# Optimization experiments

Hardware: AMD Instinct MI355X
Metric: run time of the kernel (lower is better)

The kernel has to match this reference:

```python
import jax, jax.numpy as jnp
from jax import lax
import numpy as np


def setup_inputs() -> dict:
    key = jax.random.key(0)
    ks = jax.random.split(key, 7)
    B, C, L, H, K = 64, 256, 2048, 8, 3
    return {
        "src": jax.random.normal(ks[0], (B, C, L), dtype=jnp.float32),
        "conv_w": jax.random.normal(ks[1], (H, C, K), dtype=jnp.float32) * 0.05,
        "conv_b": jax.random.normal(ks[2], (H,), dtype=jnp.float32) * 0.05,
        "bn_gamma": jnp.ones((H,), dtype=jnp.float32),
        "bn_beta": jnp.zeros((H,), dtype=jnp.float32),
        "comb_w": jax.random.normal(ks[5], (H,), dtype=jnp.float32) * 0.3,
        "comb_b": jax.random.normal(ks[6], (1,), dtype=jnp.float32) * 0.05,
        "k": 64,
    }


def reference(src, conv_w, conv_b, bn_gamma, bn_beta, comb_w, comb_b, k):
    # src: (B, C, L); conv_w: (H, C, K)
    B, C, L = src.shape
    H, _, K = conv_w.shape
    # att_conv: valid 1D conv -> (B, H, Lp), Lp = L - K + 1
    xi = lax.conv_general_dilated(src, conv_w, (1,), 'VALID',
                                  dimension_numbers=('NCH', 'OIH', 'NCH'))
    xi = xi + conv_b[None, :, None]
    # BatchNorm1d in the original runs on a batch of 1 (training mode), so
    # stats are per-sample over the length dim; biased var, eps = 1e-5.
    mu = jnp.mean(xi, axis=2, keepdims=True)
    var = jnp.var(xi, axis=2, keepdims=True)
    xn = (xi - mu) * lax.rsqrt(var + 1e-5) * bn_gamma[None, :, None] + bn_beta[None, :, None]
    Lp = xn.shape[2]
    # per-(b, h) top-k indicator; indices are detached (.data) in the original
    _, idx = lax.top_k(xn, k)  # (B, H, k)
    bidx = jnp.arange(B)[:, None, None]
    hidx = jnp.arange(H)[None, :, None]
    ind = jnp.zeros_like(xn).at[bidx, hidx, idx].set(1.0)  # (B, H, Lp)
    m = jax.nn.sigmoid(xn) * ind  # softmask, (B, H, Lp)
    # kernel_size-way shifted-padding sum: M[b,h,l] = sum_i m[b,h,l-i] -> (B, H, L)
    M = sum(jnp.pad(m, ((0, 0), (0, 0), (i, K - 1 - i))) for i in range(K))
    # combine_conv is a 1x1 conv over heads; since softmasked_src[h,c,l] =
    # src[c,l] * M[h,l] / K, the head mix commutes with the src broadcast:
    gate = jnp.einsum('h,bhl->bl', comb_w, M) / K  # (B, L)
    return src * gate[:, None, :] + comb_b[0]  # (B, C, L)
```

## Files before the change

kernel.cpp:

```cpp
#include <hip/hip_runtime.h>
#include <hip/hip_bf16.h>

#define NB 64
#define NC 256
#define NL 2048
#define NH 8
#define KW 3
#define LP (NL - KW + 1)
#define NCHUNK 8
#define CPC (NC / NCHUNK)

typedef float v4f __attribute__((ext_vector_type(4)));

__device__ __forceinline__ unsigned fkey(float x) {
  unsigned b = __float_as_uint(x);
  return (b & 0x80000000u) ? ~b : (b | 0x80000000u);
}

__global__ __launch_bounds__(256) void conv_partial(
    const float* __restrict__ src, const float* __restrict__ conv_w,
    float* __restrict__ part) {
  const int t = threadIdx.x;
  const int lane = t & 63;
  const int l0 = blockIdx.x * 1024 + t * 4;
  const int b = blockIdx.y;
  const int cc = blockIdx.z;
  const int c0 = cc * CPC;

  float acc[NH][4];
#pragma unroll
  for (int h = 0; h < NH; ++h)
#pragma unroll
    for (int j = 0; j < 4; ++j) acc[h][j] = 0.f;

  const float* sp = src + ((size_t)b * NC + c0) * NL + l0;
  const bool tail = (lane == 63) && (l0 + 5 < NL);
#pragma unroll 2
  for (int c = 0; c < CPC; ++c) {
    v4f v = *(const v4f*)sp;
    float e0 = 0.f, e1 = 0.f;
    if (tail) { e0 = sp[4]; e1 = sp[5]; }
    sp += NL;
    float n0 = __shfl_down(v.x, 1);
    float n1 = __shfl_down(v.y, 1);
    if (lane == 63) { n0 = e0; n1 = e1; }
    float s0 = v.x, s1 = v.y, s2 = v.z, s3 = v.w, s4 = n0, s5 = n1;
#pragma unroll
    for (int h = 0; h < NH; ++h) {
      const float* w = conv_w + (h * NC + c0 + c) * KW;
      const float w0 = w[0], w1 = w[1], w2 = w[2];
      acc[h][0] = fmaf(s0, w0, fmaf(s1, w1, fmaf(s2, w2, acc[h][0])));
      acc[h][1] = fmaf(s1, w0, fmaf(s2, w1, fmaf(s3, w2, acc[h][1])));
      acc[h][2] = fmaf(s2, w0, fmaf(s3, w1, fmaf(s4, w2, acc[h][2])));
      acc[h][3] = fmaf(s3, w0, fmaf(s4, w1, fmaf(s5, w2, acc[h][3])));
    }
  }
#pragma unroll
  for (int h = 0; h < NH; ++h) {
    float* pr = part + ((size_t)(b * NH + h) * NCHUNK + cc) * NL + l0;
    if (l0 + 3 < LP) {
      *(v4f*)pr = *(v4f*)acc[h];
    } else {
#pragma unroll
      for (int j = 0; j < 4; ++j)
        if (l0 + j < LP) pr[j] = acc[h][j];
    }
  }
}

__global__ __launch_bounds__(256) void select_block(
    const float* __restrict__ part, float* __restrict__ xi,
    const float* __restrict__ conv_b, const float* __restrict__ bn_gamma,
    const float* __restrict__ bn_beta, const float* __restrict__ comb_w,
    const int* __restrict__ kptr) {
  const int t = threadIdx.x;
  const int lane = t & 63, wid = t >> 6;
  const int bh = blockIdx.x;
  const int h = bh & (NH - 1);
  __shared__ float xs[LP];
  __shared__ float smp[NL + 2];
  __shared__ int hist[256];
  __shared__ float rs[8];
  __shared__ float fbc[2];
  __shared__ int irs[8];
  __shared__ int ibc[4];

  const float cb = conv_b[h];
  const float* p0 = part + (size_t)bh * NCHUNK * NL;
  float s1 = 0.f, s2 = 0.f;
  for (int i = t; i < LP; i += 256) {
    float v0 = p0[i]           + p0[i + NL];
    float v1 = p0[i + 2 * NL]  + p0[i + 3 * NL];
    float v2 = p0[i + 4 * NL]  + p0[i + 5 * NL];
    float v3 = p0[i + 6 * NL]  + p0[i + 7 * NL];
    float v = ((v0 + v1) + (v2 + v3)) + cb;
    xs[i] = v;
    s1 += v;
    s2 += v * v;
  }
#pragma unroll
  for (int off = 32; off > 0; off >>= 1) {
    s1 += __shfl_down(s1, off);
    s2 += __shfl_down(s2, off);
  }
  if (lane == 0) { rs[wid] = s1; rs[wid + 4] = s2; }
  __syncthreads();
  if (t == 0) {
    float S = rs[0] + rs[1] + rs[2] + rs[3];
    float Q = rs[4] + rs[5] + rs[6] + rs[7];
    float mu = S / (float)LP;
    float var = Q / (float)LP - mu * mu;
    float inv = rsqrtf(var + 1e-5f);
    float sc = bn_gamma[h] * inv;
    fbc[0] = sc;
    fbc[1] = bn_beta[h] - mu * sc;
  }
  __syncthreads();
  {
    const float sc = fbc[0], sh = fbc[1];
    for (int i = t; i < LP; i += 256) xs[i] = fmaf(xs[i], sc, sh);
  }
  int kk = kptr[0];
  const int ktot = kk;
  unsigned prefix = 0, pm = 0;
  for (int pass = 0; pass < 4; ++pass) {
    const int shift = 24 - 8 * pass;
    hist[t] = 0;
    __syncthreads();
    for (int i = t; i < LP; i += 256) {
      unsigned u = fkey(xs[i]);
      if ((u & pm) == prefix) atomicAdd(&hist[(u >> shift) & 255], 1);
    }
    __syncthreads();
    if (t < 64) {
      const int h0 = hist[t * 4 + 0], h1 = hist[t * 4 + 1];
      const int h2 = hist[t * 4 + 2], h3 = hist[t * 4 + 3];
      const int g = h0 + h1 + h2 + h3;
      int sfx = g;
#pragma unroll
      for (int off = 1; off < 64; off <<= 1) {
        int o = __shfl(sfx, (t + off) & 63);
        if (t + off < 64) sfx += o;
      }
      const int A = sfx - g;
      const int s3 = A + h3, s2i = s3 + h2, s1i = s2i + h1, s0i = s1i + h0;
      int mybin = -1, mykk = 0;
      if (s0i >= kk && s0i - h0 < kk) { mybin = t * 4 + 0; mykk = kk - (s0i - h0); }
      if (s1i >= kk && s1i - h1 < kk) { mybin = t * 4 + 1; mykk = kk - (s1i - h1); }
      if (s2i >= kk && s2i - h2 < kk) { mybin = t * 4 + 2; mykk = kk - (s2i - h2); }
      if (s3  >= kk && s3  - h3 < kk) { mybin = t * 4 + 3; mykk = kk - (s3 - h3); }
      if (mybin >= 0) { ibc[0] = mybin; ibc[1] = mykk; }
    }
    __syncthreads();
    prefix |= ((unsigned)ibc[0]) << shift;
    pm |= 255u << shift;
    kk = ibc[1];
  }
  const unsigned T = prefix;

  int cgt = 0, ceq = 0;
  for (int i = t; i < LP; i += 256) {
    unsigned u = fkey(xs[i]);
    cgt += (u > T);
    ceq += (u == T);
  }
#pragma unroll
  for (int off = 32; off > 0; off >>= 1) {
    cgt += __shfl_down(cgt, off);
    ceq += __shfl_down(ceq, off);
  }
  if (lane == 0) { irs[wid] = cgt; irs[wid + 4] = ceq; }
  __syncthreads();
  if (t == 0) {
    ibc[2] = irs[0] + irs[1] + irs[2] + irs[3];
    ibc[3] = irs[4] + irs[5] + irs[6] + irs[7];
  }
  __syncthreads();
  const int need_eq = ktot - ibc[2];
  const bool tie = (ibc[3] != need_eq);

  for (int i = t; i < LP; i += 256) {
    float x = xs[i];
    unsigned u = fkey(x);
    bool sel = tie ? (u > T) : (u >= T);
    smp[i + 2] = sel ? 1.f / (1.f + __expf(-x)) : 0.f;
  }
  if (t < 2) { smp[t] = 0.f; smp[NL + t] = 0.f; }
  __syncthreads();
  if (tie && t == 0) {
    int taken = 0;
    for (int i = 0; i < LP && taken < need_eq; ++i) {
      float x = xs[i];
      if (fkey(x) == T) { smp[i + 2] = 1.f / (1.f + __expf(-x)); ++taken; }
    }
  }
  __syncthreads();

  const float cw = comb_w[h] * (1.0f / (float)KW);
  float* row = xi + (size_t)bh * NL;
  for (int l = t; l < NL; l += 256)
    row[l] = cw * ((smp[l + 2] + smp[l + 1]) + smp[l]);
}

__global__ __launch_bounds__(256) void scale_gate(
    const float* __restrict__ src, const float* __restrict__ xi,
    const float* __restrict__ comb_b, float* __restrict__ out) {
  const int t = threadIdx.x;
  const int cchunk = blockIdx.x >> 7;
  const int pairidx = (blockIdx.x & 127) * 256 + t;
  const int b = pairidx >> 9;
  const int l4 = pairidx & 511;
  const float cb = comb_b[0];

  const v4f* xp = (const v4f*)(xi + (size_t)b * NH * NL) + l4;
  v4f g = xp[0];
#pragma unroll
  for (int h = 1; h < NH; ++h) g += xp[(size_t)h * (NL / 4)];

  const int c0 = cchunk * (NC / 16);
  const v4f* sp = (const v4f*)src + ((size_t)b * NC + c0) * (NL / 4) + l4;
  v4f* op = (v4f*)out + ((size_t)b * NC + c0) * (NL / 4) + l4;
#pragma unroll 4
  for (int c = 0; c < NC / 16; ++c) {
    v4f sv = sp[(size_t)c * (NL / 4)];
    v4f ov;
    ov.x = fmaf(sv.x, g.x, cb);
    ov.y = fmaf(sv.y, g.y, cb);
    ov.z = fmaf(sv.z, g.z, cb);
    ov.w = fmaf(sv.w, g.w, cb);
    __builtin_nontemporal_store(ov, op + (size_t)c * (NL / 4));
  }
}

extern "C" void kernel_launch(void* const* d_in, const int* in_sizes, int n_in,
                              void* d_out, int out_size, void* d_ws, size_t ws_size,
                              hipStream_t stream) {
  const float* src = (const float*)d_in[0];
  const float* conv_w = (const float*)d_in[1];
  const float* conv_b = (const float*)d_in[2];
  const float* bn_gamma = (const float*)d_in[3];
  const float* bn_beta = (const float*)d_in[4];
  const float* comb_w = (const float*)d_in[5];
  const float* comb_b = (const float*)d_in[6];
  const int* kptr = (const int*)d_in[7];
  float* out = (float*)d_out;

  float* xi = (float*)d_ws;
  float* part = out;

  conv_partial<<<dim3(2, NB, NCHUNK), 256, 0, stream>>>(src, conv_w, part);
  select_block<<<NB * NH, 256, 0, stream>>>(part, xi, conv_b, bn_gamma,
                                            bn_beta, comb_w, kptr);
  scale_gate<<<2048, 256, 0, stream>>>(src, xi, comb_b, out);
}
```

Before: 92.67 us.

## Double-buffer conv input rows in LDS via async global_load_lds

```diff
diff --git a/kernel.cpp b/kernel.cpp
--- a/kernel.cpp
+++ b/kernel.cpp
@@ -17,15 +17,26 @@
   return (b & 0x80000000u) ? ~b : (b | 0x80000000u);
 }
 
-__global__ __launch_bounds__(256) void conv_partial(
+__device__ __forceinline__ void async16(const float* g, float* l) {
+  __builtin_amdgcn_global_load_lds(
+      (const __attribute__((address_space(1))) unsigned int*)g,
+      (__attribute__((address_space(3))) unsigned int*)l, 16, 0, 0);
+}
+
+__global__ __launch_bounds__(256) void conv_stage(
     const float* __restrict__ src, const float* __restrict__ conv_w,
     float* __restrict__ part) {
   const int t = threadIdx.x;
   const int lane = t & 63;
-  const int l0 = blockIdx.x * 1024 + t * 4;
+  const int wv = t >> 6;
+  const int bx = blockIdx.x;
   const int b = blockIdx.y;
   const int cc = blockIdx.z;
   const int c0 = cc * CPC;
+  const int lbase = bx * 1024;
+  const int l0 = lbase + t * 4;
+
+  __shared__ float buf[2][1040];
 
   float acc[NH][4];
 #pragma unroll
@@ -33,18 +44,25 @@
 #pragma unroll
     for (int j = 0; j < 4; ++j) acc[h][j] = 0.f;
 
-  const float* sp = src + ((size_t)b * NC + c0) * NL + l0;
-  const bool tail = (lane == 63) && (l0 + 5 < NL);
-#pragma unroll 2
+  const float* grow = src + ((size_t)b * NC + c0) * NL + lbase;
+  const bool dotail = (bx == 0);
+
+  async16(grow + wv * 256 + lane * 4, &buf[0][wv * 256]);
+  if (dotail && wv == 0 && lane < 4)
+    async16(grow + 1024 + lane * 4, &buf[0][1024]);
+  __syncthreads();
+
+  int cur = 0;
   for (int c = 0; c < CPC; ++c) {
-    v4f v = *(const v4f*)sp;
-    float e0 = 0.f, e1 = 0.f;
-    if (tail) { e0 = sp[4]; e1 = sp[5]; }
-    sp += NL;
-    float n0 = __shfl_down(v.x, 1);
-    float n1 = __shfl_down(v.y, 1);
-    if (lane == 63) { n0 = e0; n1 = e1; }
-    float s0 = v.x, s1 = v.y, s2 = v.z, s3 = v.w, s4 = n0, s5 = n1;
+    if (c + 1 < CPC) {
+      const float* gn = grow + (size_t)(c + 1) * NL;
+      async16(gn + wv * 256 + lane * 4, &buf[cur ^ 1][wv * 256]);
+      if (dotail && wv == 0 && lane < 4)
+        async16(gn + 1024 + lane * 4, &buf[cur ^ 1][1024]);
+    }
+    const float* bp = &buf[cur][t * 4];
+    const float s0 = bp[0], s1 = bp[1], s2 = bp[2];
+    const float s3 = bp[3], s4 = bp[4], s5 = bp[5];
 #pragma unroll
     for (int h = 0; h < NH; ++h) {
       const float* w = conv_w + (h * NC + c0 + c) * KW;
@@ -54,7 +72,10 @@
       acc[h][2] = fmaf(s2, w0, fmaf(s3, w1, fmaf(s4, w2, acc[h][2])));
       acc[h][3] = fmaf(s3, w0, fmaf(s4, w1, fmaf(s5, w2, acc[h][3])));
     }
-  }
+    __syncthreads();
+    cur ^= 1;
+  }
+
 #pragma unroll
   for (int h = 0; h < NH; ++h) {
     float* pr = part + ((size_t)(b * NH + h) * NCHUNK + cc) * NL + l0;
@@ -248,7 +269,7 @@
   float* xi = (float*)d_ws;
   float* part = out;
 
-  conv_partial<<<dim3(2, NB, NCHUNK), 256, 0, stream>>>(src, conv_w, part);
+  conv_stage<<<dim3(2, NB, NCHUNK), 256, 0, stream>>>(src, conv_w, part);
   select_block<<<NB * NH, 256, 0, stream>>>(part, xi, conv_b, bn_gamma,
                                             bn_beta, comb_w, kptr);
   scale_gate<<<2048, 256, 0, stream>>>(src, xi, comb_b, out);
```

New measurement: 95.26 us. +2.8%, slower.
